# Kernel optimization log

Hardware: AMD Instinct MI355X
Metric: run time of the kernel (lower is better)

## Reference

```python
import jax, jax.numpy as jnp
import numpy as np

T, B, S = 32, 64, 128
V, WV, ENC, DEC, ATT = 50000, 512, 512, 512, 512
LAYERS, POOL = 2, 2
IN0 = WV + ENC  # input_feed concat


def _gru_cell(x, h, W_ih, b_ih, W_hh, b_hh):
    gi = x @ W_ih.T + b_ih
    gh = h @ W_hh.T + b_hh
    i_r, i_z, i_n = jnp.split(gi, 3, axis=-1)
    h_r, h_z, h_n = jnp.split(gh, 3, axis=-1)
    r = jax.nn.sigmoid(i_r + h_r)
    z = jax.nn.sigmoid(i_z + h_z)
    n = jnp.tanh(i_n + r * h_n)
    return (1.0 - z) * n + z * h


def setup_inputs() -> dict:
    key = jax.random.key(0)
    ks = iter(jax.random.split(key, 32))
    d = {}
    d['input'] = jax.random.randint(next(ks), (T, B), 0, V)
    d['hidden'] = jax.random.normal(next(ks), (LAYERS, B, DEC), jnp.float32)
    d['context'] = jax.random.normal(next(ks), (S, B, ENC), jnp.float32)
    d['src_pad_mask'] = jnp.zeros((B, S), jnp.float32)
    d['init_att'] = jax.random.normal(next(ks), (B, ENC), jnp.float32)
    sc = 0.05
    d['emb_W'] = jax.random.normal(next(ks), (V, WV), jnp.float32) * sc
    # stacked GRU params (layer0 input IN0, layer1 input DEC)
    d['W_ih0'] = jax.random.normal(next(ks), (3 * DEC, IN0), jnp.float32) * sc
    d['b_ih0'] = jnp.zeros((3 * DEC,), jnp.float32)
    d['W_hh0'] = jax.random.normal(next(ks), (3 * DEC, DEC), jnp.float32) * sc
    d['b_hh0'] = jnp.zeros((3 * DEC,), jnp.float32)
    d['W_ih1'] = jax.random.normal(next(ks), (3 * DEC, DEC), jnp.float32) * sc
    d['b_ih1'] = jnp.zeros((3 * DEC,), jnp.float32)
    d['W_hh1'] = jax.random.normal(next(ks), (3 * DEC, DEC), jnp.float32) * sc
    d['b_hh1'] = jnp.zeros((3 * DEC,), jnp.float32)
    # concat attention
    d['W_pre'] = jax.random.normal(next(ks), (ATT, ENC), jnp.float32) * sc
    d['b_pre'] = jnp.zeros((ATT,), jnp.float32)
    d['W_q'] = jax.random.normal(next(ks), (ATT, DEC), jnp.float32) * sc
    d['w_v'] = jax.random.normal(next(ks), (ATT,), jnp.float32) * sc
    # copy switch
    d['W_copy'] = jax.random.normal(next(ks), (1, ENC + DEC), jnp.float32) * sc
    d['b_copy'] = jnp.zeros((1,), jnp.float32)
    # readout
    d['W_read'] = jax.random.normal(next(ks), (DEC, WV + DEC + ENC), jnp.float32) * sc
    d['b_read'] = jnp.zeros((DEC,), jnp.float32)
    return d


def reference(input, hidden, context, src_pad_mask, init_att, emb_W,
              W_ih0, b_ih0, W_hh0, b_hh0, W_ih1, b_ih1, W_hh1, b_hh1,
              W_pre, b_pre, W_q, w_v, W_copy, b_copy, W_read, b_read):
    emb = emb_W[input]                     # [T,B,WV]
    ctx_bse = jnp.transpose(context, (1, 0, 2))  # [B,S,ENC]
    precompute = jnp.einsum('bse,ae->bsa', ctx_bse, W_pre) + b_pre  # [B,S,ATT]
    neg_inf = jnp.finfo(jnp.float32).min

    def step(carry, emb_t):
        h, cur_ctx = carry
        x = jnp.concatenate([emb_t, cur_ctx], axis=1)  # input_feed
        h0 = _gru_cell(x, h[0], W_ih0, b_ih0, W_hh0, b_hh0)
        out = _gru_cell(h0, h[1], W_ih1, b_ih1, W_hh1, b_hh1)
        h_new = jnp.stack([h0, out])
        # concat attention
        q = out @ W_q.T                                  # [B,ATT]
        energy = jnp.tanh(precompute + q[:, None, :]) @ w_v  # [B,S]
        energy = jnp.where(src_pad_mask > 0.5, neg_inf, energy)
        attn = jax.nn.softmax(energy, axis=-1)
        new_ctx = jnp.einsum('bs,bse->be', attn, ctx_bse)
        copy_prob = jax.nn.sigmoid(
            jnp.concatenate([out, new_ctx], axis=1) @ W_copy.T + b_copy)  # [B,1]
        readout = jnp.concatenate([emb_t, out, new_ctx], axis=1) @ W_read.T + b_read
        maxout = jnp.max(readout.reshape(B, DEC // POOL, POOL), axis=-1)  # [B,DEC/POOL]
        return (h_new, new_ctx), (maxout, attn, copy_prob)

    (hidden_f, cur_ctx_f), (g_outputs, c_outputs, copy_gates) = jax.lax.scan(
        step, (hidden, init_att), emb)
    attn_last = c_outputs[-1]
    return g_outputs, c_outputs, copy_gates, hidden_f, attn_last, cur_ctx_f
```

## Files before the change

kernel.cpp:

```cpp
#include <hip/hip_runtime.h>


typedef unsigned short u16;
typedef unsigned long long u64;
using bf16x8 = __attribute__((ext_vector_type(8))) short;
using f32x4  = __attribute__((ext_vector_type(4))) float;

#define OFF_EGI    0
#define OFF_EREAD  3145728
#define OFF_CNT    6291456
#define CNT_BYTES  101376

#define UB_PREB    8388608
#define UB_WIH0C   18087936
#define UB_WHH0    18874368
#define UB_WHH1    19660800
#define UB_WIH1    20447232
#define UB_WRO     21233664
#define UB_WRC     21495808
#define UB_CTXT    21757952
#define UB_WQ      26050560
#define ROT_H0B    26312704
#define ROT_H1B    27394048
#define ROT_CTXB   28475392

#define PH_A   0
#define PH_B   1
#define PH_CT  2

#define OO_G    0
#define OO_C    524288
#define OO_CP   786432
#define OO_HID  788480
#define OO_AL   854016
#define OO_CTXF 862208

__device__ __forceinline__ float sigm(float x) {
    return 1.0f / (1.0f + __expf(-x));
}
__device__ __forceinline__ float tanh_(float x) {
    x = fmaxf(x, -15.f);
    float e = __expf(-2.0f * x);
    return (1.0f - e) / (1.0f + e);
}
__device__ __forceinline__ u16 f2b(float x) {
    unsigned u = __float_as_uint(x);
    return (u16)((u + 0x7FFFu + ((u >> 16) & 1u)) >> 16);
}
__device__ __forceinline__ float b2f(unsigned u) {
    return __uint_as_float(u << 16);
}
__device__ __forceinline__ float bfe(bf16x8 v, int k) {
    return b2f((unsigned)(unsigned short)v[k]);
}

__device__ __forceinline__ void sta8(void* p, u64 v) {
    __hip_atomic_store((u64*)p, v, __ATOMIC_RELAXED, __HIP_MEMORY_SCOPE_AGENT);
}
__device__ __forceinline__ void sta4(void* p, unsigned v) {
    __hip_atomic_store((unsigned*)p, v, __ATOMIC_RELAXED, __HIP_MEMORY_SCOPE_AGENT);
}

__device__ __forceinline__ unsigned* cptr(float* wsf, int t, int ph, int g) {
    return (unsigned*)(wsf + OFF_CNT) + ((((t * 3) + ph) * 8 + g) << 5);
}
__device__ __forceinline__ void bar_wait1(unsigned* c, unsigned tgt) {
    if (threadIdx.x == 0) {
        while (__hip_atomic_load(c, __ATOMIC_RELAXED, __HIP_MEMORY_SCOPE_AGENT) < tgt)
            __builtin_amdgcn_s_sleep(1);
    }
    __syncthreads();
}
__device__ __forceinline__ void bar_wait8(unsigned* base, unsigned tgt) {
    if (threadIdx.x < 8) {
        unsigned* c = base + (threadIdx.x << 5);
        while (__hip_atomic_load(c, __ATOMIC_RELAXED, __HIP_MEMORY_SCOPE_AGENT) < tgt)
            __builtin_amdgcn_s_sleep(1);
    }
    __syncthreads();
}
__device__ __forceinline__ void bar_arrive(unsigned* c) {
    asm volatile("s_waitcnt vmcnt(0)" ::: "memory");
    __syncthreads();
    if (threadIdx.x == 0)
        __hip_atomic_fetch_add(c, 1u, __ATOMIC_RELAXED, __HIP_MEMORY_SCOPE_AGENT);
}

__device__ __forceinline__ void gemm64(
    const float* __restrict__ xrow, const float* __restrict__ wrow,
    int kt0, int nkt, float* lds_x, float* lds_w,
    float* __restrict__ outp, int JW, int orow0, int j0,
    const float* __restrict__ addp, int addmode, int addJW,
    u16* __restrict__ obf)
{
    const int tid = threadIdx.x;
    const int tb4 = tid >> 4, tj4 = tid & 15;
    float acc[4][4];
#pragma unroll
    for (int a = 0; a < 4; ++a)
#pragma unroll
        for (int b = 0; b < 4; ++b) acc[a][b] = 0.f;

    for (int kt = kt0; kt < kt0 + nkt; ++kt) {
        const int kb = kt << 6;
        __syncthreads();
        {
            const int rl = tid >> 2;
#pragma unroll
            for (int i = 0; i < 4; ++i) {
                const int kk = ((tid & 3) << 4) + (i << 2);
                float4 xv = *(const float4*)(xrow + kb + kk);
                float4 wv = *(const float4*)(wrow + kb + kk);
                lds_x[(kk + 0) * 64 + rl] = xv.x;
                lds_x[(kk + 1) * 64 + rl] = xv.y;
                lds_x[(kk + 2) * 64 + rl] = xv.z;
                lds_x[(kk + 3) * 64 + rl] = xv.w;
                lds_w[(kk + 0) * 64 + rl] = wv.x;
                lds_w[(kk + 1) * 64 + rl] = wv.y;
                lds_w[(kk + 2) * 64 + rl] = wv.z;
                lds_w[(kk + 3) * 64 + rl] = wv.w;
            }
        }
        __syncthreads();
#pragma unroll 4
        for (int kk = 0; kk < 64; ++kk) {
            float4 xv = *(const float4*)(lds_x + kk * 64 + tb4 * 4);
            float4 wv = *(const float4*)(lds_w + kk * 64 + tj4 * 4);
            acc[0][0] += xv.x * wv.x; acc[0][1] += xv.x * wv.y;
            acc[0][2] += xv.x * wv.z; acc[0][3] += xv.x * wv.w;
            acc[1][0] += xv.y * wv.x; acc[1][1] += xv.y * wv.y;
            acc[1][2] += xv.y * wv.z; acc[1][3] += xv.y * wv.w;
            acc[2][0] += xv.z * wv.x; acc[2][1] += xv.z * wv.y;
            acc[2][2] += xv.z * wv.z; acc[2][3] += xv.z * wv.w;
            acc[3][0] += xv.w * wv.x; acc[3][1] += xv.w * wv.y;
            acc[3][2] += xv.w * wv.z; acc[3][3] += xv.w * wv.w;
        }
    }
#pragma unroll
    for (int ib = 0; ib < 4; ++ib) {
        const int row = tb4 * 4 + ib;
        const int jc = j0 + tj4 * 4;
        float4 r;
        r.x = acc[ib][0]; r.y = acc[ib][1]; r.z = acc[ib][2]; r.w = acc[ib][3];
        if (addmode == 1) {
            float4 bv = *(const float4*)(addp + jc);
            r.x += bv.x; r.y += bv.y; r.z += bv.z; r.w += bv.w;
        } else if (addmode == 2) {
            float4 bv = *(const float4*)(addp + (size_t)(orow0 + row) * addJW + jc);
            r.x += bv.x; r.y += bv.y; r.z += bv.z; r.w += bv.w;
        }
        if (obf) {
            u64 pv = (u64)f2b(r.x) | ((u64)f2b(r.y) << 16)
                   | ((u64)f2b(r.z) << 32) | ((u64)f2b(r.w) << 48);
            *(u64*)(obf + (size_t)(orow0 + row) * 512 + jc) = pv;
        } else {
            *(float4*)(outp + (size_t)(orow0 + row) * JW + jc) = r;
        }
    }
}

__device__ __forceinline__ void stage_plain(const u16* __restrict__ Xg, u16* sX) {
    const int tid = threadIdx.x;
#pragma unroll
    for (int p = 0; p < 16; ++p) {
        const int chunk = p * 256 + tid;
        const int row = chunk >> 6, cb16 = chunk & 63;
        const int src = row * 1024 + cb16 * 16;
        const int dst = src ^ ((row & 7) << 4);
        *(float4*)((char*)sX + dst) = *(const float4*)((const char*)Xg + src);
    }
}

__device__ __forceinline__ void mfma_tile(const u16* sX, const u16* __restrict__ Wg,
                                          f32x4 acc[4]) {
    const int tid = threadIdx.x;
    const int w = tid >> 6, l15 = tid & 15, lhi = (tid & 63) >> 4;
    const int arow = w * 16 + l15;
    const char* aptr = (const char*)sX;
    const int abase = arow * 1024 + lhi * 16;
    const int aswz = (arow & 7) << 4;
#pragma unroll 4
    for (int ks = 0; ks < 16; ++ks) {
        bf16x8 a = *(const bf16x8*)(aptr + ((abase + ks * 64) ^ aswz));
        const u16* wp = Wg + l15 * 512 + ks * 32 + lhi * 8;
        acc[0] = __builtin_amdgcn_mfma_f32_16x16x32_bf16(a, *(const bf16x8*)(wp), acc[0], 0, 0, 0);
        acc[1] = __builtin_amdgcn_mfma_f32_16x16x32_bf16(a, *(const bf16x8*)(wp + 16*512), acc[1], 0, 0, 0);
        acc[2] = __builtin_amdgcn_mfma_f32_16x16x32_bf16(a, *(const bf16x8*)(wp + 32*512), acc[2], 0, 0, 0);
        acc[3] = __builtin_amdgcn_mfma_f32_16x16x32_bf16(a, *(const bf16x8*)(wp + 48*512), acc[3], 0, 0, 0);
    }
}

__device__ __forceinline__ void mfma_tile3(const u16* sX,
        const u16* __restrict__ W0, const u16* __restrict__ W1,
        const u16* __restrict__ W2, f32x4 a0[4], f32x4 a1[4], f32x4 a2[4]) {
    const int tid = threadIdx.x;
    const int w = tid >> 6, l15 = tid & 15, lhi = (tid & 63) >> 4;
    const int arow = w * 16 + l15;
    const char* aptr = (const char*)sX;
    const int abase = arow * 1024 + lhi * 16;
    const int aswz = (arow & 7) << 4;
#pragma unroll 2
    for (int ks = 0; ks < 16; ++ks) {
        bf16x8 a = *(const bf16x8*)(aptr + ((abase + ks * 64) ^ aswz));
        const int wo = l15 * 512 + ks * 32 + lhi * 8;
        const u16 *p0 = W0 + wo, *p1 = W1 + wo, *p2 = W2 + wo;
        bf16x8 b00 = *(const bf16x8*)(p0),         b01 = *(const bf16x8*)(p0 + 8192);
        bf16x8 b02 = *(const bf16x8*)(p0 + 16384), b03 = *(const bf16x8*)(p0 + 24576);
        bf16x8 b10 = *(const bf16x8*)(p1),         b11 = *(const bf16x8*)(p1 + 8192);
        bf16x8 b12 = *(const bf16x8*)(p1 + 16384), b13 = *(const bf16x8*)(p1 + 24576);
        bf16x8 b20 = *(const bf16x8*)(p2),         b21 = *(const bf16x8*)(p2 + 8192);
        bf16x8 b22 = *(const bf16x8*)(p2 + 16384), b23 = *(const bf16x8*)(p2 + 24576);
        a0[0] = __builtin_amdgcn_mfma_f32_16x16x32_bf16(a, b00, a0[0], 0, 0, 0);
        a0[1] = __builtin_amdgcn_mfma_f32_16x16x32_bf16(a, b01, a0[1], 0, 0, 0);
        a0[2] = __builtin_amdgcn_mfma_f32_16x16x32_bf16(a, b02, a0[2], 0, 0, 0);
        a0[3] = __builtin_amdgcn_mfma_f32_16x16x32_bf16(a, b03, a0[3], 0, 0, 0);
        a1[0] = __builtin_amdgcn_mfma_f32_16x16x32_bf16(a, b10, a1[0], 0, 0, 0);
        a1[1] = __builtin_amdgcn_mfma_f32_16x16x32_bf16(a, b11, a1[1], 0, 0, 0);
        a1[2] = __builtin_amdgcn_mfma_f32_16x16x32_bf16(a, b12, a1[2], 0, 0, 0);
        a1[3] = __builtin_amdgcn_mfma_f32_16x16x32_bf16(a, b13, a1[3], 0, 0, 0);
        a2[0] = __builtin_amdgcn_mfma_f32_16x16x32_bf16(a, b20, a2[0], 0, 0, 0);
        a2[1] = __builtin_amdgcn_mfma_f32_16x16x32_bf16(a, b21, a2[1], 0, 0, 0);
        a2[2] = __builtin_amdgcn_mfma_f32_16x16x32_bf16(a, b22, a2[2], 0, 0, 0);
        a2[3] = __builtin_amdgcn_mfma_f32_16x16x32_bf16(a, b23, a2[3], 0, 0, 0);
    }
}
__device__ __forceinline__ void zero4(f32x4 a[4]) {
    f32x4 z = {0.f, 0.f, 0.f, 0.f};
    a[0] = z; a[1] = z; a[2] = z; a[3] = z;
}

__global__ __launch_bounds__(256)
void k_upfront(const int* __restrict__ inp, const float* __restrict__ hid,
               const float* __restrict__ ctxin, const float* __restrict__ init_att,
               const float* __restrict__ embW,
               const float* __restrict__ W_ih0, const float* __restrict__ b_ih0,
               const float* __restrict__ W_hh0, const float* __restrict__ W_hh1,
               const float* __restrict__ W_ih1, const float* __restrict__ W_q,
               const float* __restrict__ W_read, const float* __restrict__ b_read,
               const float* __restrict__ W_pre, const float* __restrict__ b_pre,
               float* __restrict__ wsf)
{
    __shared__ float lds_x[4096], lds_w[4096];
    u16* wsu = (u16*)wsf;
    const int jid = blockIdx.x, tid = threadIdx.x, rl = tid >> 2;
    if (jid < 768) {
        const int mt = jid / 24, jt = jid % 24, j0 = jt << 6;
        const int idx = inp[mt * 64 + rl];
        gemm64(embW + (size_t)idx * 512, W_ih0 + (size_t)(j0 + rl) * 1024,
               0, 8, lds_x, lds_w, wsf + OFF_EGI, 1536, mt << 6, j0, b_ih0, 1, 0, nullptr);
    } else if (jid < 1024) {
        const int r = jid - 768, mt = r >> 3, jt = r & 7, j0 = jt << 6;
        const int idx = inp[mt * 64 + rl];
        gemm64(embW + (size_t)idx * 512, W_read + (size_t)(j0 + rl) * 1536,
               0, 8, lds_x, lds_w, wsf + OFF_EREAD, 512, mt << 6, j0, b_read, 1, 0, nullptr);
    } else if (jid < 2048) {
        const int r = jid - 1024, mt = r >> 3, jt = r & 7, j0 = jt << 6;
        const int m = (mt << 6) + rl, b = m >> 7, s = m & 127;
        gemm64(ctxin + (size_t)((s << 6) + b) * 512, W_pre + (size_t)(j0 + rl) * 512,
               0, 8, lds_x, lds_w, nullptr, 512, mt << 6, j0, b_pre, 1, 0,
               wsu + UB_PREB);
    } else if (jid < 2272) {
        const int w = jid - 2048;
        if (w < 48) {
            for (int i = 0; i < 64; ++i) {
                int e = w * 16384 + i * 256 + tid;
                int j = e >> 9, k = e & 511;
                wsu[UB_WIH0C + e] = f2b(W_ih0[(size_t)j * 1024 + 512 + k]);
            }
        } else if (w < 96) {
            for (int i = 0; i < 64; ++i) {
                int e = (w - 48) * 16384 + i * 256 + tid;
                wsu[UB_WHH0 + e] = f2b(W_hh0[e]);
            }
        } else if (w < 144) {
            for (int i = 0; i < 64; ++i) {
                int e = (w - 96) * 16384 + i * 256 + tid;
                wsu[UB_WHH1 + e] = f2b(W_hh1[e]);
            }
        } else if (w < 192) {
            for (int i = 0; i < 64; ++i) {
                int e = (w - 144) * 16384 + i * 256 + tid;
                wsu[UB_WIH1 + e] = f2b(W_ih1[e]);
            }
        } else if (w < 208) {
            for (int i = 0; i < 64; ++i) {
                int e = (w - 192) * 16384 + i * 256 + tid;
                int j = e >> 9, k = e & 511;
                wsu[UB_WRO + e] = f2b(W_read[(size_t)j * 1536 + 512 + k]);
            }
        } else {
            for (int i = 0; i < 64; ++i) {
                int e = (w - 208) * 16384 + i * 256 + tid;
                int j = e >> 9, k = e & 511;
                wsu[UB_WRC + e] = f2b(W_read[(size_t)j * 1536 + 1024 + k]);
            }
        }
    } else if (jid < 2528) {
        const int w2 = jid - 2272;
        for (int rr = 0; rr < 32; ++rr) {
            const int r = w2 * 32 + rr;
            const int b = r >> 7, s = r & 127;
            const float* src = ctxin + ((size_t)s * 64 + b) * 512;
#pragma unroll
            for (int h = 0; h < 2; ++h) {
                int e = h * 256 + tid;
                wsu[UB_CTXT + (size_t)r * 512 + e] = f2b(src[e]);
            }
        }
    } else if (jid < 2544) {
        const int w3 = jid - 2528;
        for (int i = 0; i < 64; ++i) {
            int e = w3 * 16384 + i * 256 + tid;
            wsu[UB_WQ + e] = f2b(W_q[e]);
        }
    } else {
        const int job = jid - 2544;
        const float* src = job == 0 ? hid : (job == 1 ? hid + 32768 : init_att);
        u16* dst = wsu + (size_t)(job == 0 ? ROT_H0B : (job == 1 ? ROT_H1B : ROT_CTXB))
                 + (size_t)32 * 32768;
        for (int i = 0; i < 128; ++i) {
            int e = i * 256 + tid;
            dst[e] = f2b(src[e]);
        }
    }
}

__global__ __launch_bounds__(256, 1)
void k_loop(const float* __restrict__ b_hh0, const float* __restrict__ b_ih1,
            const float* __restrict__ b_hh1, const float* __restrict__ hid,
            const float* __restrict__ maskp, const float* __restrict__ w_v,
            const float* __restrict__ W_copy, const float* __restrict__ b_copy,
            float* __restrict__ wsf, float* __restrict__ dout)
{
    __shared__ u16 sX[32768];
    u16* wsu = (u16*)wsf;
    const int blk = blockIdx.x, tid = threadIdx.x;
    const int w = tid >> 6, l15 = tid & 15, lhi = (tid & 63) >> 4;

    if (blk < 8) {
        const int j = blk;
        float hp[4][4];
#pragma unroll
        for (int cb = 0; cb < 4; ++cb)
#pragma unroll
            for (int r = 0; r < 4; ++r)
                hp[cb][r] = hid[(w * 16 + lhi * 4 + r) * 512 + j * 64 + cb * 16 + l15];

        for (int t = 0; t < 32; ++t) {
            const size_t slot = t, slotp = (t == 0) ? 32 : (size_t)(t - 1);
            float eg0[4][4], eg1[4][4], eg2[4][4];
            {
                const float* EG = wsf + OFF_EGI + (size_t)t * 98304;
#pragma unroll
                for (int cb = 0; cb < 4; ++cb) {
                    const int gc = j * 64 + cb * 16 + l15;
#pragma unroll
                    for (int r = 0; r < 4; ++r) {
                        const float* eg = EG + (size_t)(w * 16 + lhi * 4 + r) * 1536;
                        eg0[cb][r] = eg[gc];
                        eg1[cb][r] = eg[512 + gc];
                        eg2[cb][r] = eg[1024 + gc];
                    }
                }
            }
            f32x4 aR[4], aZ[4], aIN[4], aHN[4];
            zero4(aR); zero4(aZ); zero4(aIN); zero4(aHN);
            if (t > 0) bar_wait1(cptr(wsf, t - 1, PH_A, 0), 8);
            stage_plain(wsu + ROT_H0B + slotp * 32768, sX);
            __syncthreads();
            mfma_tile3(sX, wsu + UB_WHH0 + (size_t)(j * 64) * 512,
                           wsu + UB_WHH0 + (size_t)(512 + j * 64) * 512,
                           wsu + UB_WHH0 + (size_t)(1024 + j * 64) * 512, aR, aZ, aHN);
            __syncthreads();
            if (t > 0) bar_wait8(cptr(wsf, t - 1, PH_CT, 0), 8);
            stage_plain(wsu + ROT_CTXB + slotp * 32768, sX);
            __syncthreads();
            mfma_tile3(sX, wsu + UB_WIH0C + (size_t)(j * 64) * 512,
                           wsu + UB_WIH0C + (size_t)(512 + j * 64) * 512,
                           wsu + UB_WIH0C + (size_t)(1024 + j * 64) * 512, aR, aZ, aIN);
            __syncthreads();
            u16* tile = sX;
#pragma unroll
            for (int cb = 0; cb < 4; ++cb) {
                const int lc = cb * 16 + l15, gc = j * 64 + lc;
                const float brr = b_hh0[gc], bzz = b_hh0[512 + gc], bnn = b_hh0[1024 + gc];
#pragma unroll
                for (int r = 0; r < 4; ++r) {
                    const int row = w * 16 + lhi * 4 + r;
                    float rr = sigm(aR[cb][r] + eg0[cb][r] + brr);
                    float zz = sigm(aZ[cb][r] + eg1[cb][r] + bzz);
                    float nn = tanh_(aIN[cb][r] + eg2[cb][r] + rr * (aHN[cb][r] + bnn));
                    float v = (1.f - zz) * nn + zz * hp[cb][r];
                    hp[cb][r] = v;
                    tile[row * 64 + lc] = f2b(v);
                    if (t == 31) dout[OO_HID + row * 512 + gc] = v;
                }
            }
            __syncthreads();
            {
                u16* dst = wsu + ROT_H0B + slot * 32768 + j * 64;
#pragma unroll
                for (int i = 0; i < 4; ++i) {
                    int e = i * 256 + tid, row = e >> 4, c = e & 15;
                    sta8(dst + (size_t)row * 512 + c * 4, *(const u64*)(tile + row * 64 + c * 4));
                }
            }
            bar_arrive(cptr(wsf, t, PH_A, 0));
        }
    } else if (blk < 16) {
        const int j = blk - 8;
        float hp[4][4];
#pragma unroll
        for (int cb = 0; cb < 4; ++cb)
#pragma unroll
            for (int r = 0; r < 4; ++r)
                hp[cb][r] = hid[32768 + (w * 16 + lhi * 4 + r) * 512 + j * 64 + cb * 16 + l15];

        for (int t = 0; t < 32; ++t) {
            const size_t slot = t, slotp = (t == 0) ? 32 : (size_t)(t - 1);
            f32x4 aR[4], aZ[4], aIN[4], aHN[4];
            zero4(aR); zero4(aZ); zero4(aIN); zero4(aHN);
            if (t > 0) bar_wait1(cptr(wsf, t - 1, PH_B, 0), 8);
            stage_plain(wsu + ROT_H1B + slotp * 32768, sX);
            __syncthreads();
            mfma_tile3(sX, wsu + UB_WHH1 + (size_t)(j * 64) * 512,
                           wsu + UB_WHH1 + (size_t)(512 + j * 64) * 512,
                           wsu + UB_WHH1 + (size_t)(1024 + j * 64) * 512, aR, aZ, aHN);
            __syncthreads();
            bar_wait1(cptr(wsf, t, PH_A, 0), 8);
            stage_plain(wsu + ROT_H0B + slot * 32768, sX);
            __syncthreads();
            mfma_tile3(sX, wsu + UB_WIH1 + (size_t)(j * 64) * 512,
                           wsu + UB_WIH1 + (size_t)(512 + j * 64) * 512,
                           wsu + UB_WIH1 + (size_t)(1024 + j * 64) * 512, aR, aZ, aIN);
            __syncthreads();
            u16* tile = sX;
#pragma unroll
            for (int cb = 0; cb < 4; ++cb) {
                const int lc = cb * 16 + l15, gc = j * 64 + lc;
                const float bir = b_ih1[gc] + b_hh1[gc];
                const float biz = b_ih1[512 + gc] + b_hh1[512 + gc];
                const float bin_ = b_ih1[1024 + gc];
                const float bhn = b_hh1[1024 + gc];
#pragma unroll
                for (int r = 0; r < 4; ++r) {
                    const int row = w * 16 + lhi * 4 + r;
                    float rr = sigm(aR[cb][r] + bir);
                    float zz = sigm(aZ[cb][r] + biz);
                    float nn = tanh_(aIN[cb][r] + bin_ + rr * (aHN[cb][r] + bhn));
                    float v = (1.f - zz) * nn + zz * hp[cb][r];
                    hp[cb][r] = v;
                    tile[row * 64 + lc] = f2b(v);
                    if (t == 31) dout[OO_HID + 32768 + row * 512 + gc] = v;
                }
            }
            __syncthreads();
            {
                u16* dst = wsu + ROT_H1B + slot * 32768 + j * 64;
#pragma unroll
                for (int i = 0; i < 4; ++i) {
                    int e = i * 256 + tid, row = e >> 4, c = e & 15;
                    sta8(dst + (size_t)row * 512 + c * 4, *(const u64*)(tile + row * 64 + c * 4));
                }
            }
            bar_arrive(cptr(wsf, t, PH_B, 0));
        }
    } else if (blk < 80) {
        const int b = blk - 16;
        float* sf = (float*)sX;
        float* s_out  = sf;
        float* s_q    = sf + 512;
        float* s_e    = sf + 1024;
        float* s_at   = sf + 1152;
        float* s_ctx  = sf + 1280;
        float* s_red  = sf + 1792;
        float* s_part = sf + 2048;
        float* s_ctxp = sf + 2304;
        float* s_wv   = sf + 4352;
        float* s_msk  = sf + 4864;
        float* s_wcp  = sf + 4992;

        for (int i = tid; i < 512; i += 256) s_wv[i] = w_v[i];
        for (int i = tid; i < 1024; i += 256) s_wcp[i] = W_copy[i];
        if (tid < 128) s_msk[tid] = (maskp[b * 128 + tid] > 0.5f) ? -3.0e38f : 0.0f;
        __syncthreads();

        for (int t = 0; t < 32; ++t) {
            const size_t slot = t;
            bar_wait1(cptr(wsf, t, PH_B, 0), 8);
            {
                const u16* ob = wsu + ROT_H1B + slot * 32768 + b * 512;
                const int c0 = tid * 2;
                unsigned pv = *(const unsigned*)(ob + c0);
                s_out[c0] = b2f(pv & 0xffffu);
                s_out[c0 + 1] = b2f(pv >> 16);
            }
            __syncthreads();
            {
                const u16* wq0 = wsu + UB_WQ + (size_t)tid * 512;
                const u16* wq1 = wq0 + (size_t)256 * 512;
                float q0 = 0.f, q1 = 0.f;
#pragma unroll 8
                for (int i = 0; i < 64; ++i) {
                    bf16x8 w0 = *(const bf16x8*)(wq0 + i * 8);
                    bf16x8 w1 = *(const bf16x8*)(wq1 + i * 8);
#pragma unroll
                    for (int k2 = 0; k2 < 8; ++k2) {
                        float ov = s_out[i * 8 + k2];
                        q0 += ov * bfe(w0, k2);
                        q1 += ov * bfe(w1, k2);
                    }
                }
                s_q[tid] = q0; s_q[tid + 256] = q1;
            }
            __syncthreads();
            {
                const int s = tid >> 1, sh = tid & 1;
                const u16* prep = wsu + UB_PREB + (((size_t)b * 128 + s) << 9) + (sh << 8);
                float part = 0.f;
#pragma unroll 4
                for (int i = 0; i < 32; ++i) {
                    bf16x8 v = *(const bf16x8*)(prep + i * 8);
#pragma unroll
                    for (int k2 = 0; k2 < 8; ++k2) {
                        const int a = (sh << 8) + i * 8 + k2;
                        part += tanh_(bfe(v, k2) + s_q[a]) * s_wv[a];
                    }
                }
                s_part[tid] = part;
            }
            __syncthreads();
            if (tid < 128) s_e[tid] = s_part[tid * 2] + s_part[tid * 2 + 1] + s_msk[tid];
            __syncthreads();
            if (tid < 64) {
                float e0 = s_e[tid], e1 = s_e[tid + 64];
                float mx = fmaxf(e0, e1);
#pragma unroll
                for (int d2 = 1; d2 < 64; d2 <<= 1) mx = fmaxf(mx, __shfl_xor(mx, d2, 64));
                float x0 = __expf(e0 - mx), x1 = __expf(e1 - mx);
                float sm = x0 + x1;
#pragma unroll
                for (int d2 = 1; d2 < 64; d2 <<= 1) sm += __shfl_xor(sm, d2, 64);
                float inv = 1.f / sm;
                x0 *= inv; x1 *= inv;
                s_at[tid] = x0; s_at[tid + 64] = x1;
                float* co = dout + OO_C + ((size_t)t * 64 + b) * 128;
                co[tid] = x0; co[tid + 64] = x1;
                if (t == 31) {
                    dout[OO_AL + b * 128 + tid] = x0;
                    dout[OO_AL + b * 128 + tid + 64] = x1;
                }
            }
            __syncthreads();
            {
                const u16* ct = wsu + UB_CTXT + (size_t)b * 65536;
                const int ln = tid & 63;
                float ac[8] = {0.f,0.f,0.f,0.f,0.f,0.f,0.f,0.f};
#pragma unroll 4
                for (int si = 0; si < 32; ++si) {
                    const int s2 = w * 32 + si;
                    const float at = s_at[s2];
                    bf16x8 v = *(const bf16x8*)(ct + (size_t)s2 * 512 + ln * 8);
#pragma unroll
                    for (int k2 = 0; k2 < 8; ++k2) ac[k2] = fmaf(at, bfe(v, k2), ac[k2]);
                }
#pragma unroll
                for (int k2 = 0; k2 < 8; ++k2) s_ctxp[w * 512 + ln * 8 + k2] = ac[k2];
            }
            __syncthreads();
            {
                const int e0 = tid * 2;
                float c0 = s_ctxp[e0] + s_ctxp[512 + e0] + s_ctxp[1024 + e0] + s_ctxp[1536 + e0];
                float c1 = s_ctxp[e0 + 1] + s_ctxp[512 + e0 + 1] + s_ctxp[1024 + e0 + 1] + s_ctxp[1536 + e0 + 1];
                s_ctx[e0] = c0; s_ctx[e0 + 1] = c1;
                sta4(wsu + ROT_CTXB + slot * 32768 + b * 512 + e0,
                     (unsigned)f2b(c0) | ((unsigned)f2b(c1) << 16));
                if (t == 31) {
                    dout[OO_CTXF + b * 512 + e0] = c0;
                    dout[OO_CTXF + b * 512 + e0 + 1] = c1;
                }
            }
            bar_arrive(cptr(wsf, t, PH_CT, b >> 3));
            {
                const int i2 = tid * 2;
                float part = s_out[i2] * s_wcp[i2] + s_ctx[i2] * s_wcp[512 + i2]
                           + s_out[i2 + 1] * s_wcp[i2 + 1] + s_ctx[i2 + 1] * s_wcp[512 + i2 + 1];
                s_red[tid] = part;
                __syncthreads();
                for (int d2 = 128; d2 > 0; d2 >>= 1) {
                    if (tid < d2) s_red[tid] += s_red[tid + d2];
                    __syncthreads();
                }
                if (tid == 0)
                    dout[OO_CP + t * 64 + b] = sigm(s_red[0] + b_copy[0]);
            }
        }
    } else {
        const int j = blk - 80;
        for (int tp = 0; tp < 32; ++tp) {
            bar_wait1(cptr(wsf, tp, PH_B, 0), 8);
            stage_plain(wsu + ROT_H1B + (size_t)tp * 32768, sX);
            __syncthreads();
            f32x4 acc[4];
            zero4(acc);
            mfma_tile(sX, wsu + UB_WRO + (size_t)(j * 64) * 512, acc);
            bar_wait8(cptr(wsf, tp, PH_CT, 0), 8);
            __syncthreads();
            stage_plain(wsu + ROT_CTXB + (size_t)tp * 32768, sX);
            __syncthreads();
            mfma_tile(sX, wsu + UB_WRC + (size_t)(j * 64) * 512, acc);
            __syncthreads();
            float* ft = (float*)sX;
            const float* ER = wsf + OFF_EREAD + (size_t)tp * 32768;
#pragma unroll
            for (int cb = 0; cb < 4; ++cb) {
                const int lc = cb * 16 + l15;
#pragma unroll
                for (int r = 0; r < 4; ++r) {
                    const int row = w * 16 + lhi * 4 + r;
                    ft[row * 64 + lc] = acc[cb][r] + ER[(size_t)row * 512 + j * 64 + lc];
                }
            }
            __syncthreads();
#pragma unroll
            for (int i = 0; i < 8; ++i) {
                int e = i * 256 + tid, row = e >> 5, c2 = e & 31;
                dout[OO_G + (size_t)tp * 16384 + row * 256 + j * 32 + c2] =
                    fmaxf(ft[row * 64 + 2 * c2], ft[row * 64 + 2 * c2 + 1]);
            }
        }
    }
}

extern "C" void kernel_launch(void* const* d_in, const int* in_sizes, int n_in,
                              void* d_out, int out_size, void* d_ws, size_t ws_size,
                              hipStream_t stream) {
    const int*   inp      = (const int*)d_in[0];
    const float* hid      = (const float*)d_in[1];
    const float* ctxin    = (const float*)d_in[2];
    const float* maskp    = (const float*)d_in[3];
    const float* init_att = (const float*)d_in[4];
    const float* embW     = (const float*)d_in[5];
    const float* W_ih0    = (const float*)d_in[6];
    const float* b_ih0    = (const float*)d_in[7];
    const float* W_hh0    = (const float*)d_in[8];
    const float* b_hh0    = (const float*)d_in[9];
    const float* W_ih1    = (const float*)d_in[10];
    const float* b_ih1    = (const float*)d_in[11];
    const float* W_hh1    = (const float*)d_in[12];
    const float* b_hh1    = (const float*)d_in[13];
    const float* W_pre    = (const float*)d_in[14];
    const float* b_pre    = (const float*)d_in[15];
    const float* W_q      = (const float*)d_in[16];
    const float* w_v      = (const float*)d_in[17];
    const float* W_copy   = (const float*)d_in[18];
    const float* b_copy   = (const float*)d_in[19];
    const float* W_read   = (const float*)d_in[20];
    const float* b_read   = (const float*)d_in[21];
    float* dout = (float*)d_out;
    float* wsf  = (float*)d_ws;

    hipMemsetAsync((char*)d_ws + (size_t)OFF_CNT * 4, 0, CNT_BYTES, stream);

    k_upfront<<<dim3(2547), dim3(256), 0, stream>>>(
        inp, hid, ctxin, init_att, embW, W_ih0, b_ih0, W_hh0, W_hh1, W_ih1, W_q,
        W_read, b_read, W_pre, b_pre, wsf);

    k_loop<<<dim3(88), dim3(256), 0, stream>>>(
        b_hh0, b_ih1, b_hh1, hid, maskp, w_v, W_copy, b_copy, wsf, dout);
}
```

Baseline: 3.100 ms.

## Widen persistent loop blocks to 512 threads and rebalance GRU/attention work split

The persistent recurrent kernel moves from 88 blocks of 256 threads to 80 blocks of 512 threads. GRU layers now use 4 blocks each, with 128 columns per block split across 8 waves. The attention blocks keep their precompute slice in registers, use 512 threads for the query, energy and context stages, and publish the context before writing the attention outputs. The readout blocks idle half their waves during the MFMA. The aim is to shorten the per-step critical path through fewer barrier participants and more parallelism per step, at the cost of higher register pressure and underused waves in the readout blocks.

```diff
diff --git a/kernel.cpp b/kernel.cpp
--- a/kernel.cpp
+++ b/kernel.cpp
@@ -159,11 +159,11 @@
     }
 }
 
-__device__ __forceinline__ void stage_plain(const u16* __restrict__ Xg, u16* sX) {
+__device__ __forceinline__ void stage512(const u16* __restrict__ Xg, u16* sX) {
     const int tid = threadIdx.x;
 #pragma unroll
-    for (int p = 0; p < 16; ++p) {
-        const int chunk = p * 256 + tid;
+    for (int p = 0; p < 8; ++p) {
+        const int chunk = p * 512 + tid;
         const int row = chunk >> 6, cb16 = chunk & 63;
         const int src = row * 1024 + cb16 * 16;
         const int dst = src ^ ((row & 7) << 4);
@@ -171,31 +171,12 @@
     }
 }
 
-__device__ __forceinline__ void mfma_tile(const u16* sX, const u16* __restrict__ Wg,
-                                          f32x4 acc[4]) {
-    const int tid = threadIdx.x;
-    const int w = tid >> 6, l15 = tid & 15, lhi = (tid & 63) >> 4;
-    const int arow = w * 16 + l15;
-    const char* aptr = (const char*)sX;
-    const int abase = arow * 1024 + lhi * 16;
-    const int aswz = (arow & 7) << 4;
-#pragma unroll 4
-    for (int ks = 0; ks < 16; ++ks) {
-        bf16x8 a = *(const bf16x8*)(aptr + ((abase + ks * 64) ^ aswz));
-        const u16* wp = Wg + l15 * 512 + ks * 32 + lhi * 8;
-        acc[0] = __builtin_amdgcn_mfma_f32_16x16x32_bf16(a, *(const bf16x8*)(wp), acc[0], 0, 0, 0);
-        acc[1] = __builtin_amdgcn_mfma_f32_16x16x32_bf16(a, *(const bf16x8*)(wp + 16*512), acc[1], 0, 0, 0);
-        acc[2] = __builtin_amdgcn_mfma_f32_16x16x32_bf16(a, *(const bf16x8*)(wp + 32*512), acc[2], 0, 0, 0);
-        acc[3] = __builtin_amdgcn_mfma_f32_16x16x32_bf16(a, *(const bf16x8*)(wp + 48*512), acc[3], 0, 0, 0);
-    }
-}
-
-__device__ __forceinline__ void mfma_tile3(const u16* sX,
+__device__ __forceinline__ void mfma_tile3r(const u16* sX, int rb,
         const u16* __restrict__ W0, const u16* __restrict__ W1,
         const u16* __restrict__ W2, f32x4 a0[4], f32x4 a1[4], f32x4 a2[4]) {
-    const int tid = threadIdx.x;
-    const int w = tid >> 6, l15 = tid & 15, lhi = (tid & 63) >> 4;
-    const int arow = w * 16 + l15;
+    const int l = threadIdx.x & 63;
+    const int l15 = l & 15, lhi = l >> 4;
+    const int arow = rb * 16 + l15;
     const char* aptr = (const char*)sX;
     const int abase = arow * 1024 + lhi * 16;
     const int aswz = (arow & 7) << 4;
@@ -222,6 +203,24 @@
         a2[1] = __builtin_amdgcn_mfma_f32_16x16x32_bf16(a, b21, a2[1], 0, 0, 0);
         a2[2] = __builtin_amdgcn_mfma_f32_16x16x32_bf16(a, b22, a2[2], 0, 0, 0);
         a2[3] = __builtin_amdgcn_mfma_f32_16x16x32_bf16(a, b23, a2[3], 0, 0, 0);
+    }
+}
+__device__ __forceinline__ void mfma_tile4(const u16* sX, const u16* __restrict__ Wg,
+                                           f32x4 acc[4]) {
+    const int tid = threadIdx.x;
+    const int w = tid >> 6, l15 = tid & 15, lhi = (tid & 63) >> 4;
+    const int arow = w * 16 + l15;
+    const char* aptr = (const char*)sX;
+    const int abase = arow * 1024 + lhi * 16;
+    const int aswz = (arow & 7) << 4;
+#pragma unroll 4
+    for (int ks = 0; ks < 16; ++ks) {
+        bf16x8 a = *(const bf16x8*)(aptr + ((abase + ks * 64) ^ aswz));
+        const u16* wp = Wg + l15 * 512 + ks * 32 + lhi * 8;
+        acc[0] = __builtin_amdgcn_mfma_f32_16x16x32_bf16(a, *(const bf16x8*)(wp), acc[0], 0, 0, 0);
+        acc[1] = __builtin_amdgcn_mfma_f32_16x16x32_bf16(a, *(const bf16x8*)(wp + 16*512), acc[1], 0, 0, 0);
+        acc[2] = __builtin_amdgcn_mfma_f32_16x16x32_bf16(a, *(const bf16x8*)(wp + 32*512), acc[2], 0, 0, 0);
+        acc[3] = __builtin_amdgcn_mfma_f32_16x16x32_bf16(a, *(const bf16x8*)(wp + 48*512), acc[3], 0, 0, 0);
     }
 }
 __device__ __forceinline__ void zero4(f32x4 a[4]) {
@@ -325,7 +324,7 @@
     }
 }
 
-__global__ __launch_bounds__(256, 1)
+__global__ __launch_bounds__(512, 1)
 void k_loop(const float* __restrict__ b_hh0, const float* __restrict__ b_ih1,
             const float* __restrict__ b_hh1, const float* __restrict__ hid,
             const float* __restrict__ maskp, const float* __restrict__ w_v,
@@ -338,25 +337,36 @@
     const int w = tid >> 6, l15 = tid & 15, lhi = (tid & 63) >> 4;
 
     if (blk < 8) {
-        const int j = blk;
+        const bool L0 = blk < 4;
+        const int j = L0 ? blk : blk - 4;
+        const int rb = w & 3, ch = w >> 2;
+        const int lc = ch * 64;
+        const int gcol0 = j * 128 + lc;
         float hp[4][4];
 #pragma unroll
         for (int cb = 0; cb < 4; ++cb)
 #pragma unroll
             for (int r = 0; r < 4; ++r)
-                hp[cb][r] = hid[(w * 16 + lhi * 4 + r) * 512 + j * 64 + cb * 16 + l15];
+                hp[cb][r] = hid[(L0 ? 0 : 32768) +
+                                (rb * 16 + lhi * 4 + r) * 512 + gcol0 + cb * 16 + l15];
+
+        const u16* Wih = L0 ? (wsu + UB_WIH0C) : (wsu + UB_WIH1);
+        const u16* Whh = L0 ? (wsu + UB_WHH0) : (wsu + UB_WHH1);
+        const size_t rotIn  = L0 ? ROT_CTXB : ROT_H0B;
+        const size_t rotHH  = L0 ? ROT_H0B : ROT_H1B;
+        const size_t rotOut = L0 ? ROT_H0B : ROT_H1B;
 
         for (int t = 0; t < 32; ++t) {
             const size_t slot = t, slotp = (t == 0) ? 32 : (size_t)(t - 1);
             float eg0[4][4], eg1[4][4], eg2[4][4];
-            {
+            if (L0) {
                 const float* EG = wsf + OFF_EGI + (size_t)t * 98304;
 #pragma unroll
                 for (int cb = 0; cb < 4; ++cb) {
-                    const int gc = j * 64 + cb * 16 + l15;
+                    const int gc = gcol0 + cb * 16 + l15;
 #pragma unroll
                     for (int r = 0; r < 4; ++r) {
-                        const float* eg = EG + (size_t)(w * 16 + lhi * 4 + r) * 1536;
+                        const float* eg = EG + (size_t)(rb * 16 + lhi * 4 + r) * 1536;
                         eg0[cb][r] = eg[gc];
                         eg1[cb][r] = eg[512 + gc];
                         eg2[cb][r] = eg[1024 + gc];
@@ -365,131 +375,93 @@
             }
             f32x4 aR[4], aZ[4], aIN[4], aHN[4];
             zero4(aR); zero4(aZ); zero4(aIN); zero4(aHN);
-            if (t > 0) bar_wait1(cptr(wsf, t - 1, PH_A, 0), 8);
-            stage_plain(wsu + ROT_H0B + slotp * 32768, sX);
-            __syncthreads();
-            mfma_tile3(sX, wsu + UB_WHH0 + (size_t)(j * 64) * 512,
-                           wsu + UB_WHH0 + (size_t)(512 + j * 64) * 512,
-                           wsu + UB_WHH0 + (size_t)(1024 + j * 64) * 512, aR, aZ, aHN);
-            __syncthreads();
-            if (t > 0) bar_wait8(cptr(wsf, t - 1, PH_CT, 0), 8);
-            stage_plain(wsu + ROT_CTXB + slotp * 32768, sX);
-            __syncthreads();
-            mfma_tile3(sX, wsu + UB_WIH0C + (size_t)(j * 64) * 512,
-                           wsu + UB_WIH0C + (size_t)(512 + j * 64) * 512,
-                           wsu + UB_WIH0C + (size_t)(1024 + j * 64) * 512, aR, aZ, aIN);
+            if (t > 0) bar_wait1(cptr(wsf, t - 1, L0 ? PH_A : PH_B, 0), 4);
+            stage512(wsu + rotHH + slotp * 32768, sX);
+            __syncthreads();
+            mfma_tile3r(sX, rb, Whh + (size_t)gcol0 * 512,
+                                Whh + (size_t)(512 + gcol0) * 512,
+                                Whh + (size_t)(1024 + gcol0) * 512, aR, aZ, aHN);
+            __syncthreads();
+            if (L0) { if (t > 0) bar_wait8(cptr(wsf, t - 1, PH_CT, 0), 8); }
+            else    { bar_wait1(cptr(wsf, t, PH_A, 0), 4); }
+            stage512(wsu + rotIn + (L0 ? slotp : slot) * 32768, sX);
+            __syncthreads();
+            mfma_tile3r(sX, rb, Wih + (size_t)gcol0 * 512,
+                                Wih + (size_t)(512 + gcol0) * 512,
+                                Wih + (size_t)(1024 + gcol0) * 512, aR, aZ, aIN);
             __syncthreads();
             u16* tile = sX;
 #pragma unroll
             for (int cb = 0; cb < 4; ++cb) {
-                const int lc = cb * 16 + l15, gc = j * 64 + lc;
-                const float brr = b_hh0[gc], bzz = b_hh0[512 + gc], bnn = b_hh0[1024 + gc];
+                const int lcl = lc + cb * 16 + l15;
+                const int gc = j * 128 + lcl;
+                float brr, bzz, bin_, bhn;
+                if (L0) {
+                    brr = b_hh0[gc]; bzz = b_hh0[512 + gc]; bin_ = 0.f; bhn = b_hh0[1024 + gc];
+                } else {
+                    brr = b_ih1[gc] + b_hh1[gc];
+                    bzz = b_ih1[512 + gc] + b_hh1[512 + gc];
+                    bin_ = b_ih1[1024 + gc];
+                    bhn = b_hh1[1024 + gc];
+                }
 #pragma unroll
                 for (int r = 0; r < 4; ++r) {
-                    const int row = w * 16 + lhi * 4 + r;
-                    float rr = sigm(aR[cb][r] + eg0[cb][r] + brr);
-                    float zz = sigm(aZ[cb][r] + eg1[cb][r] + bzz);
-                    float nn = tanh_(aIN[cb][r] + eg2[cb][r] + rr * (aHN[cb][r] + bnn));
+                    const int row = rb * 16 + lhi * 4 + r;
+                    float ir = aR[cb][r] + (L0 ? eg0[cb][r] : 0.f) + brr;
+                    float iz = aZ[cb][r] + (L0 ? eg1[cb][r] : 0.f) + bzz;
+                    float inn = aIN[cb][r] + (L0 ? eg2[cb][r] : 0.f) + bin_;
+                    float rr = sigm(ir), zz = sigm(iz);
+                    float nn = tanh_(inn + rr * (aHN[cb][r] + bhn));
                     float v = (1.f - zz) * nn + zz * hp[cb][r];
                     hp[cb][r] = v;
-                    tile[row * 64 + lc] = f2b(v);
-                    if (t == 31) dout[OO_HID + row * 512 + gc] = v;
+                    tile[row * 128 + lcl] = f2b(v);
+                    if (t == 31) dout[OO_HID + (L0 ? 0 : 32768) + row * 512 + gc] = v;
                 }
             }
             __syncthreads();
             {
-                u16* dst = wsu + ROT_H0B + slot * 32768 + j * 64;
+                u16* dst = wsu + rotOut + slot * 32768 + j * 128;
 #pragma unroll
                 for (int i = 0; i < 4; ++i) {
-                    int e = i * 256 + tid, row = e >> 4, c = e & 15;
-                    sta8(dst + (size_t)row * 512 + c * 4, *(const u64*)(tile + row * 64 + c * 4));
-                }
-            }
-            bar_arrive(cptr(wsf, t, PH_A, 0));
-        }
-    } else if (blk < 16) {
-        const int j = blk - 8;
-        float hp[4][4];
-#pragma unroll
-        for (int cb = 0; cb < 4; ++cb)
-#pragma unroll
-            for (int r = 0; r < 4; ++r)
-                hp[cb][r] = hid[32768 + (w * 16 + lhi * 4 + r) * 512 + j * 64 + cb * 16 + l15];
-
-        for (int t = 0; t < 32; ++t) {
-            const size_t slot = t, slotp = (t == 0) ? 32 : (size_t)(t - 1);
-            f32x4 aR[4], aZ[4], aIN[4], aHN[4];
-            zero4(aR); zero4(aZ); zero4(aIN); zero4(aHN);
-            if (t > 0) bar_wait1(cptr(wsf, t - 1, PH_B, 0), 8);
-            stage_plain(wsu + ROT_H1B + slotp * 32768, sX);
-            __syncthreads();
-            mfma_tile3(sX, wsu + UB_WHH1 + (size_t)(j * 64) * 512,
-                           wsu + UB_WHH1 + (size_t)(512 + j * 64) * 512,
-                           wsu + UB_WHH1 + (size_t)(1024 + j * 64) * 512, aR, aZ, aHN);
-            __syncthreads();
-            bar_wait1(cptr(wsf, t, PH_A, 0), 8);
-            stage_plain(wsu + ROT_H0B + slot * 32768, sX);
-            __syncthreads();
-            mfma_tile3(sX, wsu + UB_WIH1 + (size_t)(j * 64) * 512,
-                           wsu + UB_WIH1 + (size_t)(512 + j * 64) * 512,
-                           wsu + UB_WIH1 + (size_t)(1024 + j * 64) * 512, aR, aZ, aIN);
-            __syncthreads();
-            u16* tile = sX;
-#pragma unroll
-            for (int cb = 0; cb < 4; ++cb) {
-                const int lc = cb * 16 + l15, gc = j * 64 + lc;
-                const float bir = b_ih1[gc] + b_hh1[gc];
-                const float biz = b_ih1[512 + gc] + b_hh1[512 + gc];
-                const float bin_ = b_ih1[1024 + gc];
-                const float bhn = b_hh1[1024 + gc];
-#pragma unroll
-                for (int r = 0; r < 4; ++r) {
-                    const int row = w * 16 + lhi * 4 + r;
-                    float rr = sigm(aR[cb][r] + bir);
-                    float zz = sigm(aZ[cb][r] + biz);
-                    float nn = tanh_(aIN[cb][r] + bin_ + rr * (aHN[cb][r] + bhn));
-                    float v = (1.f - zz) * nn + zz * hp[cb][r];
-                    hp[cb][r] = v;
-                    tile[row * 64 + lc] = f2b(v);
-                    if (t == 31) dout[OO_HID + 32768 + row * 512 + gc] = v;
-                }
-            }
-            __syncthreads();
-            {
-                u16* dst = wsu + ROT_H1B + slot * 32768 + j * 64;
-#pragma unroll
-                for (int i = 0; i < 4; ++i) {
-                    int e = i * 256 + tid, row = e >> 4, c = e & 15;
-                    sta8(dst + (size_t)row * 512 + c * 4, *(const u64*)(tile + row * 64 + c * 4));
-                }
-            }
-            bar_arrive(cptr(wsf, t, PH_B, 0));
-        }
-    } else if (blk < 80) {
-        const int b = blk - 16;
+                    int e = i * 512 + tid;
+                    int row = e >> 5, c8 = e & 31;
+                    sta8(dst + (size_t)row * 512 + c8 * 4,
+                         *(const u64*)(tile + row * 128 + c8 * 4));
+                }
+            }
+            bar_arrive(cptr(wsf, t, L0 ? PH_A : PH_B, 0));
+        }
+    } else if (blk < 72) {
+        const int b = blk - 8;
         float* sf = (float*)sX;
         float* s_out  = sf;
         float* s_q    = sf + 512;
         float* s_e    = sf + 1024;
         float* s_at   = sf + 1152;
-        float* s_ctx  = sf + 1280;
-        float* s_red  = sf + 1792;
-        float* s_part = sf + 2048;
-        float* s_ctxp = sf + 2304;
-        float* s_wv   = sf + 4352;
-        float* s_msk  = sf + 4864;
-        float* s_wcp  = sf + 4992;
-
-        for (int i = tid; i < 512; i += 256) s_wv[i] = w_v[i];
-        for (int i = tid; i < 1024; i += 256) s_wcp[i] = W_copy[i];
+        float* s_part = sf + 1280;
+        float* s_ctxp = sf + 1792;
+        float* s_ctx  = sf + 5888;
+        float* s_red  = sf + 6400;
+        float* s_wv   = sf + 6912;
+        float* s_msk  = sf + 7424;
+        float* s_wcp  = sf + 7552;
+
+        if (tid < 512) s_wv[tid] = w_v[tid];
+        for (int i = tid; i < 1024; i += 512) s_wcp[i] = W_copy[i];
         if (tid < 128) s_msk[tid] = (maskp[b * 128 + tid] > 0.5f) ? -3.0e38f : 0.0f;
+        const int se = tid >> 2, qu = tid & 3;
+        bf16x8 pr[16];
+        {
+            const u16* prep = wsu + UB_PREB + (((size_t)b * 128 + se) << 9) + (qu << 7);
+#pragma unroll
+            for (int i = 0; i < 16; ++i) pr[i] = *(const bf16x8*)(prep + i * 8);
+        }
         __syncthreads();
 
         for (int t = 0; t < 32; ++t) {
-            const size_t slot = t;
-            bar_wait1(cptr(wsf, t, PH_B, 0), 8);
-            {
-                const u16* ob = wsu + ROT_H1B + slot * 32768 + b * 512;
+            bar_wait1(cptr(wsf, t, PH_B, 0), 4);
+            if (tid < 256) {
+                const u16* ob = wsu + ROT_H1B + (size_t)t * 32768 + b * 512;
                 const int c0 = tid * 2;
                 unsigned pv = *(const unsigned*)(ob + c0);
                 s_out[c0] = b2f(pv & 0xffffu);
@@ -497,40 +469,35 @@
             }
             __syncthreads();
             {
-                const u16* wq0 = wsu + UB_WQ + (size_t)tid * 512;
-                const u16* wq1 = wq0 + (size_t)256 * 512;
-                float q0 = 0.f, q1 = 0.f;
+                const u16* wq = wsu + UB_WQ + (size_t)tid * 512;
+                float q = 0.f;
 #pragma unroll 8
                 for (int i = 0; i < 64; ++i) {
-                    bf16x8 w0 = *(const bf16x8*)(wq0 + i * 8);
-                    bf16x8 w1 = *(const bf16x8*)(wq1 + i * 8);
+                    bf16x8 wv8 = *(const bf16x8*)(wq + i * 8);
+#pragma unroll
+                    for (int k2 = 0; k2 < 8; ++k2)
+                        q = fmaf(s_out[i * 8 + k2], bfe(wv8, k2), q);
+                }
+                s_q[tid] = q;
+            }
+            __syncthreads();
+            {
+                float part = 0.f;
+#pragma unroll
+                for (int i = 0; i < 16; ++i) {
+                    bf16x8 v = pr[i];
 #pragma unroll
                     for (int k2 = 0; k2 < 8; ++k2) {
-                        float ov = s_out[i * 8 + k2];
-                        q0 += ov * bfe(w0, k2);
-                        q1 += ov * bfe(w1, k2);
-                    }
-                }
-                s_q[tid] = q0; s_q[tid + 256] = q1;
-            }
-            __syncthreads();
-            {
-                const int s = tid >> 1, sh = tid & 1;
-                const u16* prep = wsu + UB_PREB + (((size_t)b * 128 + s) << 9) + (sh << 8);
-                float part = 0.f;
-#pragma unroll 4
-                for (int i = 0; i < 32; ++i) {
-                    bf16x8 v = *(const bf16x8*)(prep + i * 8);
-#pragma unroll
-                    for (int k2 = 0; k2 < 8; ++k2) {
-                        const int a = (sh << 8) + i * 8 + k2;
+                        const int a = (qu << 7) + i * 8 + k2;
                         part += tanh_(bfe(v, k2) + s_q[a]) * s_wv[a];
                     }
                 }
                 s_part[tid] = part;
             }
             __syncthreads();
-            if (tid < 128) s_e[tid] = s_part[tid * 2] + s_part[tid * 2 + 1] + s_msk[tid];
+            if (tid < 128)
+                s_e[tid] = s_part[tid * 4] + s_part[tid * 4 + 1]
+                         + s_part[tid * 4 + 2] + s_part[tid * 4 + 3] + s_msk[tid];
             __syncthreads();
             if (tid < 64) {
                 float e0 = s_e[tid], e1 = s_e[tid + 64];
@@ -542,23 +509,16 @@
 #pragma unroll
                 for (int d2 = 1; d2 < 64; d2 <<= 1) sm += __shfl_xor(sm, d2, 64);
                 float inv = 1.f / sm;
-                x0 *= inv; x1 *= inv;
-                s_at[tid] = x0; s_at[tid + 64] = x1;
-                float* co = dout + OO_C + ((size_t)t * 64 + b) * 128;
-                co[tid] = x0; co[tid + 64] = x1;
-                if (t == 31) {
-                    dout[OO_AL + b * 128 + tid] = x0;
-                    dout[OO_AL + b * 128 + tid + 64] = x1;
-                }
+                s_at[tid] = x0 * inv; s_at[tid + 64] = x1 * inv;
             }
             __syncthreads();
             {
                 const u16* ct = wsu + UB_CTXT + (size_t)b * 65536;
                 const int ln = tid & 63;
                 float ac[8] = {0.f,0.f,0.f,0.f,0.f,0.f,0.f,0.f};
-#pragma unroll 4
-                for (int si = 0; si < 32; ++si) {
-                    const int s2 = w * 32 + si;
+#pragma unroll
+                for (int si = 0; si < 16; ++si) {
+                    const int s2 = w * 16 + si;
                     const float at = s_at[s2];
                     bf16x8 v = *(const bf16x8*)(ct + (size_t)s2 * 512 + ln * 8);
 #pragma unroll
@@ -568,26 +528,37 @@
                 for (int k2 = 0; k2 < 8; ++k2) s_ctxp[w * 512 + ln * 8 + k2] = ac[k2];
             }
             __syncthreads();
+            if (tid < 256) {
+                const int e0 = tid * 2;
+                float c0 = 0.f, c1 = 0.f;
+#pragma unroll
+                for (int ww = 0; ww < 8; ++ww) {
+                    c0 += s_ctxp[ww * 512 + e0];
+                    c1 += s_ctxp[ww * 512 + e0 + 1];
+                }
+                s_ctx[e0] = c0; s_ctx[e0 + 1] = c1;
+                sta4(wsu + ROT_CTXB + (size_t)t * 32768 + b * 512 + e0,
+                     (unsigned)f2b(c0) | ((unsigned)f2b(c1) << 16));
+            }
+            bar_arrive(cptr(wsf, t, PH_CT, b >> 3));
+            if (tid < 64) {
+                float* co = dout + OO_C + ((size_t)t * 64 + b) * 128;
+                co[tid] = s_at[tid]; co[tid + 64] = s_at[tid + 64];
+                if (t == 31) {
+                    dout[OO_AL + b * 128 + tid] = s_at[tid];
+                    dout[OO_AL + b * 128 + tid + 64] = s_at[tid + 64];
+                }
+            }
+            if (t == 31 && tid < 256) {
+                const int e0 = tid * 2;
+                dout[OO_CTXF + b * 512 + e0] = s_ctx[e0];
+                dout[OO_CTXF + b * 512 + e0 + 1] = s_ctx[e0 + 1];
+            }
             {
-                const int e0 = tid * 2;
-                float c0 = s_ctxp[e0] + s_ctxp[512 + e0] + s_ctxp[1024 + e0] + s_ctxp[1536 + e0];
-                float c1 = s_ctxp[e0 + 1] + s_ctxp[512 + e0 + 1] + s_ctxp[1024 + e0 + 1] + s_ctxp[1536 + e0 + 1];
-                s_ctx[e0] = c0; s_ctx[e0 + 1] = c1;
-                sta4(wsu + ROT_CTXB + slot * 32768 + b * 512 + e0,
-                     (unsigned)f2b(c0) | ((unsigned)f2b(c1) << 16));
-                if (t == 31) {
-                    dout[OO_CTXF + b * 512 + e0] = c0;
-                    dout[OO_CTXF + b * 512 + e0 + 1] = c1;
-                }
-            }
-            bar_arrive(cptr(wsf, t, PH_CT, b >> 3));
-            {
-                const int i2 = tid * 2;
-                float part = s_out[i2] * s_wcp[i2] + s_ctx[i2] * s_wcp[512 + i2]
-                           + s_out[i2 + 1] * s_wcp[i2 + 1] + s_ctx[i2 + 1] * s_wcp[512 + i2 + 1];
+                float part = s_out[tid] * s_wcp[tid] + s_ctx[tid] * s_wcp[512 + tid];
                 s_red[tid] = part;
                 __syncthreads();
-                for (int d2 = 128; d2 > 0; d2 >>= 1) {
+                for (int d2 = 256; d2 > 0; d2 >>= 1) {
                     if (tid < d2) s_red[tid] += s_red[tid + d2];
                     __syncthreads();
                 }
@@ -596,38 +567,41 @@
             }
         }
     } else {
-        const int j = blk - 80;
+        const int j = blk - 72;
         for (int tp = 0; tp < 32; ++tp) {
-            bar_wait1(cptr(wsf, tp, PH_B, 0), 8);
-            stage_plain(wsu + ROT_H1B + (size_t)tp * 32768, sX);
+            bar_wait1(cptr(wsf, tp, PH_B, 0), 4);
+            stage512(wsu + ROT_H1B + (size_t)tp * 32768, sX);
             __syncthreads();
             f32x4 acc[4];
             zero4(acc);
-            mfma_tile(sX, wsu + UB_WRO + (size_t)(j * 64) * 512, acc);
+            if (w < 4) mfma_tile4(sX, wsu + UB_WRO + (size_t)(j * 64) * 512, acc);
             bar_wait8(cptr(wsf, tp, PH_CT, 0), 8);
             __syncthreads();
-            stage_plain(wsu + ROT_CTXB + (size_t)tp * 32768, sX);
-            __syncthreads();
-            mfma_tile(sX, wsu + UB_WRC + (size_t)(j * 64) * 512, acc);
+            stage512(wsu + ROT_CTXB + (size_t)tp * 32768, sX);
+            __syncthreads();
+            if (w < 4) mfma_tile4(sX, wsu + UB_WRC + (size_t)(j * 64) * 512, acc);
             __syncthreads();
             float* ft = (float*)sX;
-            const float* ER = wsf + OFF_EREAD + (size_t)tp * 32768;
-#pragma unroll
-            for (int cb = 0; cb < 4; ++cb) {
-                const int lc = cb * 16 + l15;
-#pragma unroll
-                for (int r = 0; r < 4; ++r) {
-                    const int row = w * 16 + lhi * 4 + r;
-                    ft[row * 64 + lc] = acc[cb][r] + ER[(size_t)row * 512 + j * 64 + lc];
-                }
-            }
-            __syncthreads();
-#pragma unroll
-            for (int i = 0; i < 8; ++i) {
-                int e = i * 256 + tid, row = e >> 5, c2 = e & 31;
+            if (w < 4) {
+                const float* ER = wsf + OFF_EREAD + (size_t)tp * 32768;
+#pragma unroll
+                for (int cb = 0; cb < 4; ++cb) {
+                    const int lc = cb * 16 + l15;
+#pragma unroll
+                    for (int r = 0; r < 4; ++r) {
+                        const int row = w * 16 + lhi * 4 + r;
+                        ft[row * 64 + lc] = acc[cb][r] + ER[(size_t)row * 512 + j * 64 + lc];
+                    }
+                }
+            }
+            __syncthreads();
+#pragma unroll
+            for (int i = 0; i < 4; ++i) {
+                int e = i * 512 + tid, row = e >> 5, c2 = e & 31;
                 dout[OO_G + (size_t)tp * 16384 + row * 256 + j * 32 + c2] =
                     fmaxf(ft[row * 64 + 2 * c2], ft[row * 64 + 2 * c2 + 1]);
             }
+            __syncthreads();
         }
     }
 }
@@ -666,6 +640,6 @@
         inp, hid, ctxin, init_att, embW, W_ih0, b_ih0, W_hh0, W_hh1, W_ih1, W_q,
         W_read, b_read, W_pre, b_pre, wsf);
 
-    k_loop<<<dim3(88), dim3(256), 0, stream>>>(
+    k_loop<<<dim3(80), dim3(512), 0, stream>>>(
         b_hh0, b_ih1, b_hh1, hid, maskp, w_v, W_copy, b_copy, wsf, dout);
 }
```

After: 4.470 ms. 1.44x slower.
